# Optimization experiments

Hardware: AMD Instinct MI355X
Metric: run time of the kernel (lower is better)

The kernel has to match this reference:

```python
import jax, jax.numpy as jnp
import numpy as np

LN_EPS = 1e-5
LOG_EPS = 1e-8

def _layernorm(x, w, b):
    mu = jnp.mean(x, axis=-1, keepdims=True)
    var = jnp.mean((x - mu) ** 2, axis=-1, keepdims=True)
    return (x - mu) * jax.lax.rsqrt(var + LN_EPS) * w + b


def setup_inputs() -> dict:
    key = jax.random.key(0)
    ks = jax.random.split(key, 8)
    B, T, D = 4, 4096, 1024
    x = jax.random.normal(ks[0], (B, T, D), dtype=jnp.float32)
    ln_w = jnp.ones((D,), jnp.float32)
    ln_b = jnp.zeros((D,), jnp.float32)
    # torch Linear stores weight as (out, in)
    Wf = jax.random.normal(ks[1], (D, D), jnp.float32) / np.sqrt(D)
    bf = jax.random.normal(ks[2], (D,), jnp.float32) * 0.02
    # module inits reach to zeros; use small random values for a non-trivial baseline
    Wr = jax.random.normal(ks[3], (D, D), jnp.float32) * 0.02
    br = jax.random.normal(ks[4], (D,), jnp.float32) * 0.02
    alpha_bias = jnp.array([3.0], jnp.float32) + jax.random.normal(ks[5], (1,), jnp.float32) * 0.1
    beta_scale = jnp.array([0.02], jnp.float32)
    return {"x": x, "ln_w": ln_w, "ln_b": ln_b, "Wf": Wf, "bf": bf,
            "Wr": Wr, "br": br, "alpha_bias": alpha_bias, "beta_scale": beta_scale}


def reference(x, ln_w, ln_b, Wf, bf, Wr, br, alpha_bias, beta_scale):
    residual = x
    x_norm = _layernorm(x, ln_w, ln_b)                       # [B,T,D]
    alpha = jax.nn.sigmoid(jnp.einsum('btd,ed->bte', x_norm, Wf) + bf + alpha_bias)
    beta_x = beta_scale * (1.0 - alpha) * x_norm
    log_alpha = jnp.log(alpha + LOG_EPS)
    log_alpha_cumsum = jnp.cumsum(log_alpha, axis=1)          # [B,T,D]
    m = jnp.max(log_alpha_cumsum, axis=1, keepdims=True)      # [B,1,D]
    scale = jnp.exp(log_alpha_cumsum - m)
    x_star = beta_x * scale
    s_star = jnp.cumsum(x_star, axis=1)
    output = s_star / (scale + LOG_EPS)
    x_gate = jnp.tanh(jnp.einsum('btd,ed->bte', output, Wr) + br)
    return x_gate * 0.05 + residual
```

## Files before the change

### kernel.cpp

```cpp
#include <hip/hip_runtime.h>

#define D_DIM 1024
#define B_DIM 4
#define T_DIM 4096
#define M_DIM (B_DIM * T_DIM)
#define CHUNK 32
#define NCHUNK (T_DIM / CHUNK)
#define NWAVE_C 16
#define SEG (NCHUNK / NWAVE_C)

typedef unsigned short u16;
typedef __attribute__((ext_vector_type(8))) unsigned short us8;
typedef __attribute__((ext_vector_type(8))) __bf16 bf16x8;
typedef __attribute__((ext_vector_type(4))) float f32x4;

__device__ __forceinline__ float bf2f(u16 u) {
    union { unsigned int i; float f; } v;
    v.i = ((unsigned int)u) << 16;
    return v.f;
}
__device__ __forceinline__ u16 f2bf(float f) {
    union { float f; unsigned int i; } v;
    v.f = f;
    unsigned int u = v.i;
    unsigned int r = (u + 0x7fffu + ((u >> 16) & 1u)) >> 16;
    return (u16)r;
}
__device__ __forceinline__ float fast_tanh(float v) {
    float e = __expf(2.f * v);
    return 1.f - 2.f / (e + 1.f);
}

#define GLOAD16(g, l)                                                   \
    __builtin_amdgcn_global_load_lds(                                   \
        (const __attribute__((address_space(1))) void*)(g),             \
        (__attribute__((address_space(3))) void*)(l), 16, 0, 0)

__global__ __launch_bounds__(256) void ln_conv_kernel(const float* __restrict__ x,
                                                      const float* __restrict__ w,
                                                      const float* __restrict__ b,
                                                      u16* __restrict__ xn,
                                                      const float* __restrict__ Wf,
                                                      const float* __restrict__ Wr,
                                                      u16* __restrict__ da,
                                                      u16* __restrict__ db) {
    __shared__ float red[8];
    int tid = threadIdx.x;
    if (blockIdx.x < 2048) {
        int i = blockIdx.x * 256 + tid;
        const float* s = (i < 262144) ? Wf : Wr;
        u16* dp = (i < 262144) ? da : db;
        int j = i & 262143;
        float4 v = ((const float4*)s)[j];
        ushort4 o;
        o.x = f2bf(v.x); o.y = f2bf(v.y); o.z = f2bf(v.z); o.w = f2bf(v.w);
        ((ushort4*)dp)[j] = o;
        return;
    }
    int row = blockIdx.x - 2048;
    float4 v = ((const float4*)(x + (size_t)row * D_DIM))[tid];
    float s  = v.x + v.y + v.z + v.w;
    float s2 = v.x * v.x + v.y * v.y + v.z * v.z + v.w * v.w;
    #pragma unroll
    for (int o = 32; o > 0; o >>= 1) {
        s  += __shfl_xor(s, o, 64);
        s2 += __shfl_xor(s2, o, 64);
    }
    int wave = tid >> 6, lane = tid & 63;
    if (lane == 0) { red[wave] = s; red[wave + 4] = s2; }
    __syncthreads();
    if (tid == 0) {
        float ts  = red[0] + red[1] + red[2] + red[3];
        float ts2 = red[4] + red[5] + red[6] + red[7];
        float mu  = ts * (1.0f / D_DIM);
        float var = ts2 * (1.0f / D_DIM) - mu * mu;
        red[0] = mu;
        red[1] = rsqrtf(var + 1e-5f);
    }
    __syncthreads();
    float mu = red[0], rs = red[1];
    float4 wv = ((const float4*)w)[tid];
    float4 bv = ((const float4*)b)[tid];
    ushort4 o;
    o.x = f2bf((v.x - mu) * rs * wv.x + bv.x);
    o.y = f2bf((v.y - mu) * rs * wv.y + bv.y);
    o.z = f2bf((v.z - mu) * rs * wv.z + bv.z);
    o.w = f2bf((v.w - mu) * rs * wv.w + bv.w);
    ((ushort4*)(xn + (size_t)row * D_DIM))[tid] = o;
}

template <int EPI>
__global__ __launch_bounds__(256) void gemm_kernel(const u16* __restrict__ A,
                                                   const u16* __restrict__ Bm,
                                                   const float* __restrict__ bias,
                                                   const float* __restrict__ resid,
                                                   const float* __restrict__ sc0,
                                                   u16* __restrict__ out_bf,
                                                   float* __restrict__ out_f) {
    __shared__ __align__(16) u16 lds_a[128 * 32];
    __shared__ __align__(16) u16 lds_b[128 * 32];
    int tid  = threadIdx.x;
    int wave = tid >> 6, lane = tid & 63;
    int tile_n = blockIdx.x * 128;
    int tile_m = blockIdx.y * 128;
    int wr = wave >> 1, wc = wave & 1;

    f32x4 acc[4][4] = {};

    int srow = wave * 32 + (lane >> 2);
    int scol = (lane & 3) * 8;
    const u16* ga0 = A  + (size_t)(tile_m + srow) * D_DIM + scol;
    const u16* ga1 = ga0 + 16 * D_DIM;
    const u16* gb0 = Bm + (size_t)(tile_n + srow) * D_DIM + scol;
    const u16* gb1 = gb0 + 16 * D_DIM;
    u16* la0 = &lds_a[(wave * 32) * 32];
    u16* la1 = &lds_a[(wave * 32 + 16) * 32];
    u16* lb0 = &lds_b[(wave * 32) * 32];
    u16* lb1 = &lds_b[(wave * 32 + 16) * 32];

    for (int k0 = 0; k0 < D_DIM; k0 += 32) {
        GLOAD16(ga0 + k0, la0);
        GLOAD16(ga1 + k0, la1);
        GLOAD16(gb0 + k0, lb0);
        GLOAD16(gb1 + k0, lb1);
        __syncthreads();

        bf16x8 af[4], bfr[4];
        #pragma unroll
        for (int mi = 0; mi < 4; mi++) {
            int m = wr * 64 + mi * 16 + (lane & 15);
            af[mi] = *(const bf16x8*)&lds_a[m * 32 + (lane >> 4) * 8];
        }
        #pragma unroll
        for (int ni = 0; ni < 4; ni++) {
            int n = wc * 64 + ni * 16 + (lane & 15);
            bfr[ni] = *(const bf16x8*)&lds_b[n * 32 + (lane >> 4) * 8];
        }
        #pragma unroll
        for (int mi = 0; mi < 4; mi++)
            #pragma unroll
            for (int ni = 0; ni < 4; ni++)
                acc[mi][ni] = __builtin_amdgcn_mfma_f32_16x16x32_bf16(
                    af[mi], bfr[ni], acc[mi][ni], 0, 0, 0);
        __syncthreads();
    }

    if constexpr (EPI == 0) {
        float abv = sc0[0];
        #pragma unroll
        for (int mi = 0; mi < 4; mi++) {
            #pragma unroll
            for (int r = 0; r < 4; r++) {
                int row = tile_m + wr * 64 + mi * 16 + (lane >> 4) * 4 + r;
                #pragma unroll
                for (int ni = 0; ni < 4; ni++) {
                    int col = tile_n + wc * 64 + ni * 16 + (lane & 15);
                    size_t idx = (size_t)row * D_DIM + col;
                    float z = acc[mi][ni][r] + bias[col] + abv;
                    float alpha = 1.f / (1.f + __expf(-z));
                    out_bf[idx] = f2bf(__logf(alpha + 1e-8f));
                }
            }
        }
    } else {
        #pragma unroll
        for (int mi = 0; mi < 4; mi++) {
            #pragma unroll
            for (int r = 0; r < 4; r++) {
                int row = tile_m + wr * 64 + mi * 16 + (lane >> 4) * 4 + r;
                #pragma unroll
                for (int ni = 0; ni < 4; ni++) {
                    int col = tile_n + wc * 64 + ni * 16 + (lane & 15);
                    size_t idx = (size_t)row * D_DIM + col;
                    float g = fast_tanh(acc[mi][ni][r] + bias[col]);
                    out_f[idx] = 0.05f * g + resid[idx];
                }
            }
        }
    }
}

__global__ __launch_bounds__(256) void scan_chunk(const u16* __restrict__ la,
                                                  const u16* __restrict__ xn,
                                                  const float* __restrict__ bs,
                                                  float* __restrict__ S,
                                                  float* __restrict__ Ml,
                                                  float* __restrict__ Tb) {
    int bc = blockIdx.x;
    int b = bc >> 7, c = bc & (NCHUNK - 1);
    int col0 = threadIdx.x * 4;
    float bsv = bs[0];
    size_t base = ((size_t)(b * T_DIM + c * CHUNK)) * D_DIM + col0;
    float run[4], mx[4];
    #pragma unroll
    for (int j = 0; j < 4; j++) { run[j] = 0.f; mx[j] = -3.4e38f; }
    #pragma unroll 4
    for (int t = 0; t < CHUNK; t++) {
        ushort4 v = *(const ushort4*)(la + base + (size_t)t * D_DIM);
        run[0] += bf2f(v.x); mx[0] = fmaxf(mx[0], run[0]);
        run[1] += bf2f(v.y); mx[1] = fmaxf(mx[1], run[1]);
        run[2] += bf2f(v.z); mx[2] = fmaxf(mx[2], run[2]);
        run[3] += bf2f(v.w); mx[3] = fmaxf(mx[3], run[3]);
    }
    float tb[4], p[4];
    #pragma unroll
    for (int j = 0; j < 4; j++) { tb[j] = 0.f; p[j] = 0.f; }
    #pragma unroll 4
    for (int t = 0; t < CHUNK; t++) {
        size_t idx = base + (size_t)t * D_DIM;
        ushort4 lv = *(const ushort4*)(la + idx);
        ushort4 xv = *(const ushort4*)(xn + idx);
        u16 lvs[4] = {lv.x, lv.y, lv.z, lv.w};
        u16 xvs[4] = {xv.x, xv.y, xv.z, xv.w};
        #pragma unroll
        for (int j = 0; j < 4; j++) {
            float lav = bf2f(lvs[j]);
            p[j] += lav;
            float bx = bsv * (1.f - __expf(lav)) * bf2f(xvs[j]);
            tb[j] += bx * __expf(p[j] - mx[j]);
        }
    }
    size_t ci = ((size_t)(b * NCHUNK + c)) * D_DIM + col0;
    #pragma unroll
    for (int j = 0; j < 4; j++) { S[ci + j] = run[j]; Ml[ci + j] = mx[j]; Tb[ci + j] = tb[j]; }
}

__global__ __launch_bounds__(1024) void scan_combine(const float* __restrict__ S,
                                                     const float* __restrict__ Ml,
                                                     const float* __restrict__ Tb,
                                                     float* __restrict__ Of,
                                                     float* __restrict__ SSp) {
    __shared__ float lsS[NWAVE_C][64], lsM[NWAVE_C][64], lsW[NWAVE_C][64];
    int b = blockIdx.x >> 4;
    int dg = blockIdx.x & 15;
    int wave = threadIdx.x >> 6, lane = threadIdx.x & 63;
    int d = dg * 64 + lane;
    size_t base = ((size_t)b * NCHUNK) * D_DIM + d;
    int c0 = wave * SEG;

    float O = 0.f, m = -3.4e38f;
    #pragma unroll
    for (int j = 0; j < SEG; j++) {
        size_t ci = base + (size_t)(c0 + j) * D_DIM;
        m = fmaxf(m, O + Ml[ci]);
        O += S[ci];
    }
    lsS[wave][lane] = O; lsM[wave][lane] = m;
    __syncthreads();

    float myOsup = 0.f, gm = -3.4e38f;
    {
        float o = 0.f;
        #pragma unroll
        for (int w2 = 0; w2 < NWAVE_C; w2++) {
            if (w2 == wave) myOsup = o;
            gm = fmaxf(gm, o + lsM[w2][lane]);
            o += lsS[w2][lane];
        }
    }

    float wv[SEG];
    float wacc = 0.f, Oc = myOsup;
    #pragma unroll
    for (int j = 0; j < SEG; j++) {
        size_t ci = base + (size_t)(c0 + j) * D_DIM;
        Of[ci] = Oc - gm;
        float wcj = __expf(Oc + Ml[ci] - gm) * Tb[ci];
        wv[j] = wacc;
        wacc += wcj;
        Oc += S[ci];
    }
    lsW[wave][lane] = wacc;
    __syncthreads();

    float ssup = 0.f;
    #pragma unroll
    for (int w2 = 0; w2 < NWAVE_C; w2++)
        if (w2 < wave) ssup += lsW[w2][lane];

    #pragma unroll
    for (int j = 0; j < SEG; j++) {
        size_t ci = base + (size_t)(c0 + j) * D_DIM;
        SSp[ci] = ssup + wv[j];
    }
}

__global__ __launch_bounds__(256) void scan_final(const u16* __restrict__ la,
                                                  const u16* __restrict__ xn,
                                                  const float* __restrict__ bs,
                                                  const float* __restrict__ Of,
                                                  const float* __restrict__ SSp,
                                                  u16* __restrict__ osc) {
    int bc = blockIdx.x;
    int b = bc >> 7, c = bc & (NCHUNK - 1);
    int col0 = threadIdx.x * 4;
    float bsv = bs[0];
    size_t base = ((size_t)(b * T_DIM + c * CHUNK)) * D_DIM + col0;
    size_t ci = ((size_t)(b * NCHUNK + c)) * D_DIM + col0;
    float ofs[4], ss[4], p[4];
    #pragma unroll
    for (int j = 0; j < 4; j++) { ofs[j] = Of[ci + j]; ss[j] = SSp[ci + j]; p[j] = 0.f; }
    #pragma unroll 4
    for (int t = 0; t < CHUNK; t++) {
        size_t idx = base + (size_t)t * D_DIM;
        ushort4 lv = *(const ushort4*)(la + idx);
        ushort4 xv = *(const ushort4*)(xn + idx);
        u16 lvs[4] = {lv.x, lv.y, lv.z, lv.w};
        u16 xvs[4] = {xv.x, xv.y, xv.z, xv.w};
        ushort4 o;
        u16 os[4];
        #pragma unroll
        for (int j = 0; j < 4; j++) {
            float lav = bf2f(lvs[j]);
            p[j] += lav;
            float scv = __expf(ofs[j] + p[j]);
            float bx = bsv * (1.f - __expf(lav)) * bf2f(xvs[j]);
            ss[j] += bx * scv;
            os[j] = f2bf(ss[j] / (scv + 1e-8f));
        }
        o.x = os[0]; o.y = os[1]; o.z = os[2]; o.w = os[3];
        *(ushort4*)(osc + idx) = o;
    }
}

extern "C" void kernel_launch(void* const* d_in, const int* in_sizes, int n_in,
                              void* d_out, int out_size, void* d_ws, size_t ws_size,
                              hipStream_t stream) {
    const float* x   = (const float*)d_in[0];
    const float* lnw = (const float*)d_in[1];
    const float* lnb = (const float*)d_in[2];
    const float* Wf  = (const float*)d_in[3];
    const float* bf_ = (const float*)d_in[4];
    const float* Wr  = (const float*)d_in[5];
    const float* br  = (const float*)d_in[6];
    const float* ab  = (const float*)d_in[7];
    const float* bs  = (const float*)d_in[8];
    float* out = (float*)d_out;

    char* w = (char*)d_ws;
    u16* xn  = (u16*)w;
    u16* la  = (u16*)(w + (size_t)33554432);
    u16* Wfc = (u16*)(w + (size_t)67108864);
    u16* Wrc = (u16*)(w + (size_t)69206016);
    float* S   = (float*)(w + (size_t)71303168);
    float* Ml  = S  + 524288;
    float* Tb  = Ml + 524288;
    float* Of  = Tb + 524288;
    float* SSp = Of + 524288;
    u16* osc = xn;

    ln_conv_kernel<<<dim3(2048 + M_DIM), dim3(256), 0, stream>>>(
        x, lnw, lnb, xn, Wf, Wr, Wfc, Wrc);
    gemm_kernel<0><<<dim3(D_DIM / 128, M_DIM / 128), dim3(256), 0, stream>>>(
        xn, Wfc, bf_, nullptr, ab, la, nullptr);
    scan_chunk<<<dim3(B_DIM * NCHUNK), dim3(256), 0, stream>>>(la, xn, bs, S, Ml, Tb);
    scan_combine<<<dim3(B_DIM * 16), dim3(1024), 0, stream>>>(S, Ml, Tb, Of, SSp);
    scan_final<<<dim3(B_DIM * NCHUNK), dim3(256), 0, stream>>>(la, xn, bs, Of, SSp, osc);
    gemm_kernel<1><<<dim3(D_DIM / 128, M_DIM / 128), dim3(256), 0, stream>>>(
        osc, Wrc, br, x, nullptr, nullptr, out);
}
```

Measured before the change: 308.1 us.

## Fuse chunk-scan summaries into first GEMM epilogue and simplify scan combine

The first GEMM epilogue now computes per-chunk sums of log-alpha and the weighted beta_x totals directly from accumulator registers, using cross-lane shuffles, and writes them out. This removes the separate scan_chunk kernel and its two extra passes over la and xn. The per-chunk max is replaced by using the first row's log-alpha as the stabilising offset, which drops the Ml buffer but could lose numerical stability if the cumulative sums drift far from that value. LayerNorm is also restructured to one row per wave, with shuffle-only reductions and no block syncs.

```diff
diff --git a/kernel.cpp b/kernel.cpp
--- a/kernel.cpp
+++ b/kernel.cpp
@@ -10,7 +10,6 @@
 #define SEG (NCHUNK / NWAVE_C)
 
 typedef unsigned short u16;
-typedef __attribute__((ext_vector_type(8))) unsigned short us8;
 typedef __attribute__((ext_vector_type(8))) __bf16 bf16x8;
 typedef __attribute__((ext_vector_type(4))) float f32x4;
 
@@ -44,7 +43,6 @@
                                                       const float* __restrict__ Wr,
                                                       u16* __restrict__ da,
                                                       u16* __restrict__ db) {
-    __shared__ float red[8];
     int tid = threadIdx.x;
     if (blockIdx.x < 2048) {
         int i = blockIdx.x * 256 + tid;
@@ -57,46 +55,49 @@
         ((ushort4*)dp)[j] = o;
         return;
     }
-    int row = blockIdx.x - 2048;
-    float4 v = ((const float4*)(x + (size_t)row * D_DIM))[tid];
-    float s  = v.x + v.y + v.z + v.w;
-    float s2 = v.x * v.x + v.y * v.y + v.z * v.z + v.w * v.w;
-    #pragma unroll
-    for (int o = 32; o > 0; o >>= 1) {
+    int wv = tid >> 6, lane = tid & 63;
+    int row = (blockIdx.x - 2048) * 4 + wv;
+    const float4* xr = (const float4*)(x + (size_t)row * D_DIM);
+    float4 xv[4];
+    #pragma unroll
+    for (int k = 0; k < 4; k++) xv[k] = xr[lane + 64 * k];
+    float s = 0.f, s2 = 0.f;
+    #pragma unroll
+    for (int k = 0; k < 4; k++) {
+        s  += xv[k].x + xv[k].y + xv[k].z + xv[k].w;
+        s2 += xv[k].x * xv[k].x + xv[k].y * xv[k].y
+            + xv[k].z * xv[k].z + xv[k].w * xv[k].w;
+    }
+    #pragma unroll
+    for (int o = 1; o < 64; o <<= 1) {
         s  += __shfl_xor(s, o, 64);
         s2 += __shfl_xor(s2, o, 64);
     }
-    int wave = tid >> 6, lane = tid & 63;
-    if (lane == 0) { red[wave] = s; red[wave + 4] = s2; }
-    __syncthreads();
-    if (tid == 0) {
-        float ts  = red[0] + red[1] + red[2] + red[3];
-        float ts2 = red[4] + red[5] + red[6] + red[7];
-        float mu  = ts * (1.0f / D_DIM);
-        float var = ts2 * (1.0f / D_DIM) - mu * mu;
-        red[0] = mu;
-        red[1] = rsqrtf(var + 1e-5f);
-    }
-    __syncthreads();
-    float mu = red[0], rs = red[1];
-    float4 wv = ((const float4*)w)[tid];
-    float4 bv = ((const float4*)b)[tid];
-    ushort4 o;
-    o.x = f2bf((v.x - mu) * rs * wv.x + bv.x);
-    o.y = f2bf((v.y - mu) * rs * wv.y + bv.y);
-    o.z = f2bf((v.z - mu) * rs * wv.z + bv.z);
-    o.w = f2bf((v.w - mu) * rs * wv.w + bv.w);
-    ((ushort4*)(xn + (size_t)row * D_DIM))[tid] = o;
-}
-
-template <int EPI>
-__global__ __launch_bounds__(256) void gemm_kernel(const u16* __restrict__ A,
-                                                   const u16* __restrict__ Bm,
-                                                   const float* __restrict__ bias,
-                                                   const float* __restrict__ resid,
-                                                   const float* __restrict__ sc0,
-                                                   u16* __restrict__ out_bf,
-                                                   float* __restrict__ out_f) {
+    float mu = s * (1.0f / D_DIM);
+    float var = s2 * (1.0f / D_DIM) - mu * mu;
+    float rs = rsqrtf(var + 1e-5f);
+    ushort4* xo = (ushort4*)(xn + (size_t)row * D_DIM);
+    #pragma unroll
+    for (int k = 0; k < 4; k++) {
+        float4 wv4 = ((const float4*)w)[lane + 64 * k];
+        float4 bv4 = ((const float4*)b)[lane + 64 * k];
+        ushort4 o;
+        o.x = f2bf((xv[k].x - mu) * rs * wv4.x + bv4.x);
+        o.y = f2bf((xv[k].y - mu) * rs * wv4.y + bv4.y);
+        o.z = f2bf((xv[k].z - mu) * rs * wv4.z + bv4.z);
+        o.w = f2bf((xv[k].w - mu) * rs * wv4.w + bv4.w);
+        xo[lane + 64 * k] = o;
+    }
+}
+
+__global__ __launch_bounds__(256) void gemm1_kernel(const u16* __restrict__ xn,
+                                                    const u16* __restrict__ Wfc,
+                                                    const float* __restrict__ bf_,
+                                                    const float* __restrict__ ab,
+                                                    const float* __restrict__ bs,
+                                                    u16* __restrict__ out_la,
+                                                    float* __restrict__ Sg,
+                                                    float* __restrict__ Tg) {
     __shared__ __align__(16) u16 lds_a[128 * 32];
     __shared__ __align__(16) u16 lds_b[128 * 32];
     int tid  = threadIdx.x;
@@ -104,14 +105,13 @@
     int tile_n = blockIdx.x * 128;
     int tile_m = blockIdx.y * 128;
     int wr = wave >> 1, wc = wave & 1;
-
     f32x4 acc[4][4] = {};
 
     int srow = wave * 32 + (lane >> 2);
     int scol = (lane & 3) * 8;
-    const u16* ga0 = A  + (size_t)(tile_m + srow) * D_DIM + scol;
+    const u16* ga0 = xn  + (size_t)(tile_m + srow) * D_DIM + scol;
     const u16* ga1 = ga0 + 16 * D_DIM;
-    const u16* gb0 = Bm + (size_t)(tile_n + srow) * D_DIM + scol;
+    const u16* gb0 = Wfc + (size_t)(tile_n + srow) * D_DIM + scol;
     const u16* gb1 = gb0 + 16 * D_DIM;
     u16* la0 = &lds_a[(wave * 32) * 32];
     u16* la1 = &lds_a[(wave * 32 + 16) * 32];
@@ -124,7 +124,6 @@
         GLOAD16(gb0 + k0, lb0);
         GLOAD16(gb1 + k0, lb1);
         __syncthreads();
-
         bf16x8 af[4], bfr[4];
         #pragma unroll
         for (int mi = 0; mi < 4; mi++) {
@@ -145,143 +144,98 @@
         __syncthreads();
     }
 
-    if constexpr (EPI == 0) {
-        float abv = sc0[0];
-        #pragma unroll
-        for (int mi = 0; mi < 4; mi++) {
-            #pragma unroll
-            for (int r = 0; r < 4; r++) {
-                int row = tile_m + wr * 64 + mi * 16 + (lane >> 4) * 4 + r;
+    float abv = ab[0], bsv = bs[0];
+    int q = lane >> 4, l = lane & 15;
+    #pragma unroll
+    for (int ni = 0; ni < 4; ni++) {
+        int col = tile_n + wc * 64 + ni * 16 + l;
+        float bcol = bf_[col];
+        #pragma unroll
+        for (int ch = 0; ch < 2; ch++) {
+            float lav[2][4], bxv[2][4];
+            #pragma unroll
+            for (int h = 0; h < 2; h++) {
+                int mi = 2 * ch + h;
                 #pragma unroll
-                for (int ni = 0; ni < 4; ni++) {
-                    int col = tile_n + wc * 64 + ni * 16 + (lane & 15);
-                    size_t idx = (size_t)row * D_DIM + col;
-                    float z = acc[mi][ni][r] + bias[col] + abv;
+                for (int r = 0; r < 4; r++) {
+                    int row = tile_m + wr * 64 + mi * 16 + q * 4 + r;
+                    float z = acc[mi][ni][r] + bcol + abv;
                     float alpha = 1.f / (1.f + __expf(-z));
-                    out_bf[idx] = f2bf(__logf(alpha + 1e-8f));
+                    float la_ = __logf(alpha + 1e-8f);
+                    float xv = bf2f(xn[(size_t)row * D_DIM + col]);
+                    lav[h][r] = la_;
+                    bxv[h][r] = bsv * (1.f - alpha) * xv;
+                    out_la[(size_t)row * D_DIM + col] = f2bf(la_);
                 }
             }
-        }
-    } else {
-        #pragma unroll
-        for (int mi = 0; mi < 4; mi++) {
-            #pragma unroll
-            for (int r = 0; r < 4; r++) {
-                int row = tile_m + wr * 64 + mi * 16 + (lane >> 4) * 4 + r;
-                #pragma unroll
-                for (int ni = 0; ni < 4; ni++) {
-                    int col = tile_n + wc * 64 + ni * 16 + (lane & 15);
-                    size_t idx = (size_t)row * D_DIM + col;
-                    float g = fast_tanh(acc[mi][ni][r] + bias[col]);
-                    out_f[idx] = 0.05f * g + resid[idx];
-                }
+            float s0 = lav[0][0] + lav[0][1] + lav[0][2] + lav[0][3];
+            float s1 = lav[1][0] + lav[1][1] + lav[1][2] + lav[1][3];
+            float x0 = s0, x1 = s1, y;
+            y = __shfl_up(x0, 16, 64); if (q >= 1) x0 += y;
+            y = __shfl_up(x0, 32, 64); if (q >= 2) x0 += y;
+            y = __shfl_up(x1, 16, 64); if (q >= 1) x1 += y;
+            y = __shfl_up(x1, 32, 64); if (q >= 2) x1 += y;
+            float t0 = __shfl(x0, l + 48, 64);
+            float t1 = __shfl(x1, l + 48, 64);
+            float e0 = x0 - s0, e1 = x1 - s1;
+            float pr = e0, Tp = 0.f;
+            #pragma unroll
+            for (int r = 0; r < 4; r++) { pr += lav[0][r]; Tp += bxv[0][r] * __expf(pr); }
+            pr = t0 + e1;
+            #pragma unroll
+            for (int r = 0; r < 4; r++) { pr += lav[1][r]; Tp += bxv[1][r] * __expf(pr); }
+            Tp += __shfl_xor(Tp, 16, 64);
+            Tp += __shfl_xor(Tp, 32, 64);
+            if (q == 0) {
+                int cidx = (tile_m >> 5) + wr * 2 + ch;
+                Sg[(size_t)cidx * D_DIM + col] = t0 + t1;
+                Tg[(size_t)cidx * D_DIM + col] = Tp;
             }
         }
     }
 }
 
-__global__ __launch_bounds__(256) void scan_chunk(const u16* __restrict__ la,
-                                                  const u16* __restrict__ xn,
-                                                  const float* __restrict__ bs,
-                                                  float* __restrict__ S,
-                                                  float* __restrict__ Ml,
-                                                  float* __restrict__ Tb) {
-    int bc = blockIdx.x;
-    int b = bc >> 7, c = bc & (NCHUNK - 1);
-    int col0 = threadIdx.x * 4;
-    float bsv = bs[0];
-    size_t base = ((size_t)(b * T_DIM + c * CHUNK)) * D_DIM + col0;
-    float run[4], mx[4];
-    #pragma unroll
-    for (int j = 0; j < 4; j++) { run[j] = 0.f; mx[j] = -3.4e38f; }
-    #pragma unroll 4
-    for (int t = 0; t < CHUNK; t++) {
-        ushort4 v = *(const ushort4*)(la + base + (size_t)t * D_DIM);
-        run[0] += bf2f(v.x); mx[0] = fmaxf(mx[0], run[0]);
-        run[1] += bf2f(v.y); mx[1] = fmaxf(mx[1], run[1]);
-        run[2] += bf2f(v.z); mx[2] = fmaxf(mx[2], run[2]);
-        run[3] += bf2f(v.w); mx[3] = fmaxf(mx[3], run[3]);
-    }
-    float tb[4], p[4];
-    #pragma unroll
-    for (int j = 0; j < 4; j++) { tb[j] = 0.f; p[j] = 0.f; }
-    #pragma unroll 4
-    for (int t = 0; t < CHUNK; t++) {
-        size_t idx = base + (size_t)t * D_DIM;
-        ushort4 lv = *(const ushort4*)(la + idx);
-        ushort4 xv = *(const ushort4*)(xn + idx);
-        u16 lvs[4] = {lv.x, lv.y, lv.z, lv.w};
-        u16 xvs[4] = {xv.x, xv.y, xv.z, xv.w};
-        #pragma unroll
-        for (int j = 0; j < 4; j++) {
-            float lav = bf2f(lvs[j]);
-            p[j] += lav;
-            float bx = bsv * (1.f - __expf(lav)) * bf2f(xvs[j]);
-            tb[j] += bx * __expf(p[j] - mx[j]);
-        }
-    }
-    size_t ci = ((size_t)(b * NCHUNK + c)) * D_DIM + col0;
-    #pragma unroll
-    for (int j = 0; j < 4; j++) { S[ci + j] = run[j]; Ml[ci + j] = mx[j]; Tb[ci + j] = tb[j]; }
-}
-
-__global__ __launch_bounds__(1024) void scan_combine(const float* __restrict__ S,
-                                                     const float* __restrict__ Ml,
+__global__ __launch_bounds__(1024) void scan_combine(const u16* __restrict__ la,
+                                                     const float* __restrict__ S,
                                                      const float* __restrict__ Tb,
                                                      float* __restrict__ Of,
                                                      float* __restrict__ SSp) {
-    __shared__ float lsS[NWAVE_C][64], lsM[NWAVE_C][64], lsW[NWAVE_C][64];
+    __shared__ float lsS[NWAVE_C][64], lsW[NWAVE_C][64];
     int b = blockIdx.x >> 4;
     int dg = blockIdx.x & 15;
     int wave = threadIdx.x >> 6, lane = threadIdx.x & 63;
     int d = dg * 64 + lane;
+    float m = bf2f(la[(size_t)(b * T_DIM) * D_DIM + d]);
     size_t base = ((size_t)b * NCHUNK) * D_DIM + d;
     int c0 = wave * SEG;
 
-    float O = 0.f, m = -3.4e38f;
+    float OfR[SEG], wR[SEG];
+    float Or = 0.f, w = 0.f;
     #pragma unroll
     for (int j = 0; j < SEG; j++) {
         size_t ci = base + (size_t)(c0 + j) * D_DIM;
-        m = fmaxf(m, O + Ml[ci]);
-        O += S[ci];
-    }
-    lsS[wave][lane] = O; lsM[wave][lane] = m;
+        OfR[j] = Or;
+        wR[j]  = w;
+        w  += __expf(Or) * Tb[ci];
+        Or += S[ci];
+    }
+    lsS[wave][lane] = Or; lsW[wave][lane] = w;
     __syncthreads();
 
-    float myOsup = 0.f, gm = -3.4e38f;
-    {
-        float o = 0.f;
-        #pragma unroll
-        for (int w2 = 0; w2 < NWAVE_C; w2++) {
-            if (w2 == wave) myOsup = o;
-            gm = fmaxf(gm, o + lsM[w2][lane]);
-            o += lsS[w2][lane];
-        }
-    }
-
-    float wv[SEG];
-    float wacc = 0.f, Oc = myOsup;
+    float o = 0.f, s = 0.f, myO = 0.f, myS = 0.f;
+    #pragma unroll
+    for (int w2 = 0; w2 < NWAVE_C; w2++) {
+        if (w2 == wave) { myO = o; myS = s; }
+        s += __expf(o - m) * lsW[w2][lane];
+        o += lsS[w2][lane];
+    }
+
+    float em = __expf(myO - m);
     #pragma unroll
     for (int j = 0; j < SEG; j++) {
         size_t ci = base + (size_t)(c0 + j) * D_DIM;
-        Of[ci] = Oc - gm;
-        float wcj = __expf(Oc + Ml[ci] - gm) * Tb[ci];
-        wv[j] = wacc;
-        wacc += wcj;
-        Oc += S[ci];
-    }
-    lsW[wave][lane] = wacc;
-    __syncthreads();
-
-    float ssup = 0.f;
-    #pragma unroll
-    for (int w2 = 0; w2 < NWAVE_C; w2++)
-        if (w2 < wave) ssup += lsW[w2][lane];
-
-    #pragma unroll
-    for (int j = 0; j < SEG; j++) {
-        size_t ci = base + (size_t)(c0 + j) * D_DIM;
-        SSp[ci] = ssup + wv[j];
+        Of[ci]  = myO + OfR[j] - m;
+        SSp[ci] = myS + em * wR[j];
     }
 }
 
@@ -300,14 +254,13 @@
     float ofs[4], ss[4], p[4];
     #pragma unroll
     for (int j = 0; j < 4; j++) { ofs[j] = Of[ci + j]; ss[j] = SSp[ci + j]; p[j] = 0.f; }
-    #pragma unroll 4
+    #pragma unroll 8
     for (int t = 0; t < CHUNK; t++) {
         size_t idx = base + (size_t)t * D_DIM;
         ushort4 lv = *(const ushort4*)(la + idx);
         ushort4 xv = *(const ushort4*)(xn + idx);
         u16 lvs[4] = {lv.x, lv.y, lv.z, lv.w};
         u16 xvs[4] = {xv.x, xv.y, xv.z, xv.w};
-        ushort4 o;
         u16 os[4];
         #pragma unroll
         for (int j = 0; j < 4; j++) {
@@ -318,8 +271,72 @@
             ss[j] += bx * scv;
             os[j] = f2bf(ss[j] / (scv + 1e-8f));
         }
-        o.x = os[0]; o.y = os[1]; o.z = os[2]; o.w = os[3];
+        ushort4 o; o.x = os[0]; o.y = os[1]; o.z = os[2]; o.w = os[3];
         *(ushort4*)(osc + idx) = o;
+    }
+}
+
+__global__ __launch_bounds__(256) void gemm2_kernel(const u16* __restrict__ A,
+                                                    const u16* __restrict__ Bm,
+                                                    const float* __restrict__ bias,
+                                                    const float* __restrict__ resid,
+                                                    float* __restrict__ out_f) {
+    __shared__ __align__(16) u16 lds_a[128 * 32];
+    __shared__ __align__(16) u16 lds_b[128 * 32];
+    int tid  = threadIdx.x;
+    int wave = tid >> 6, lane = tid & 63;
+    int tile_n = blockIdx.x * 128;
+    int tile_m = blockIdx.y * 128;
+    int wr = wave >> 1, wc = wave & 1;
+    f32x4 acc[4][4] = {};
+    int srow = wave * 32 + (lane >> 2);
+    int scol = (lane & 3) * 8;
+    const u16* ga0 = A  + (size_t)(tile_m + srow) * D_DIM + scol;
+    const u16* ga1 = ga0 + 16 * D_DIM;
+    const u16* gb0 = Bm + (size_t)(tile_n + srow) * D_DIM + scol;
+    const u16* gb1 = gb0 + 16 * D_DIM;
+    u16* la0 = &lds_a[(wave * 32) * 32];
+    u16* la1 = &lds_a[(wave * 32 + 16) * 32];
+    u16* lb0 = &lds_b[(wave * 32) * 32];
+    u16* lb1 = &lds_b[(wave * 32 + 16) * 32];
+    for (int k0 = 0; k0 < D_DIM; k0 += 32) {
+        GLOAD16(ga0 + k0, la0);
+        GLOAD16(ga1 + k0, la1);
+        GLOAD16(gb0 + k0, lb0);
+        GLOAD16(gb1 + k0, lb1);
+        __syncthreads();
+        bf16x8 af[4], bfr[4];
+        #pragma unroll
+        for (int mi = 0; mi < 4; mi++) {
+            int m = wr * 64 + mi * 16 + (lane & 15);
+            af[mi] = *(const bf16x8*)&lds_a[m * 32 + (lane >> 4) * 8];
+        }
+        #pragma unroll
+        for (int ni = 0; ni < 4; ni++) {
+            int n = wc * 64 + ni * 16 + (lane & 15);
+            bfr[ni] = *(const bf16x8*)&lds_b[n * 32 + (lane >> 4) * 8];
+        }
+        #pragma unroll
+        for (int mi = 0; mi < 4; mi++)
+            #pragma unroll
+            for (int ni = 0; ni < 4; ni++)
+                acc[mi][ni] = __builtin_amdgcn_mfma_f32_16x16x32_bf16(
+                    af[mi], bfr[ni], acc[mi][ni], 0, 0, 0);
+        __syncthreads();
+    }
+    #pragma unroll
+    for (int mi = 0; mi < 4; mi++) {
+        #pragma unroll
+        for (int r = 0; r < 4; r++) {
+            int row = tile_m + wr * 64 + mi * 16 + (lane >> 4) * 4 + r;
+            #pragma unroll
+            for (int ni = 0; ni < 4; ni++) {
+                int col = tile_n + wc * 64 + ni * 16 + (lane & 15);
+                size_t idx = (size_t)row * D_DIM + col;
+                float g = fast_tanh(acc[mi][ni][r] + bias[col]);
+                out_f[idx] = 0.05f * g + resid[idx];
+            }
+        }
     }
 }
 
@@ -343,19 +360,17 @@
     u16* Wfc = (u16*)(w + (size_t)67108864);
     u16* Wrc = (u16*)(w + (size_t)69206016);
     float* S   = (float*)(w + (size_t)71303168);
-    float* Ml  = S  + 524288;
-    float* Tb  = Ml + 524288;
+    float* Tb  = S  + 524288;
     float* Of  = Tb + 524288;
     float* SSp = Of + 524288;
     u16* osc = xn;
 
-    ln_conv_kernel<<<dim3(2048 + M_DIM), dim3(256), 0, stream>>>(
+    ln_conv_kernel<<<dim3(2048 + M_DIM / 4), dim3(256), 0, stream>>>(
         x, lnw, lnb, xn, Wf, Wr, Wfc, Wrc);
-    gemm_kernel<0><<<dim3(D_DIM / 128, M_DIM / 128), dim3(256), 0, stream>>>(
-        xn, Wfc, bf_, nullptr, ab, la, nullptr);
-    scan_chunk<<<dim3(B_DIM * NCHUNK), dim3(256), 0, stream>>>(la, xn, bs, S, Ml, Tb);
-    scan_combine<<<dim3(B_DIM * 16), dim3(1024), 0, stream>>>(S, Ml, Tb, Of, SSp);
+    gemm1_kernel<<<dim3(D_DIM / 128, M_DIM / 128), dim3(256), 0, stream>>>(
+        xn, Wfc, bf_, ab, bs, la, S, Tb);
+    scan_combine<<<dim3(B_DIM * 16), dim3(1024), 0, stream>>>(la, S, Tb, Of, SSp);
     scan_final<<<dim3(B_DIM * NCHUNK), dim3(256), 0, stream>>>(la, xn, bs, Of, SSp, osc);
-    gemm_kernel<1><<<dim3(D_DIM / 128, M_DIM / 128), dim3(256), 0, stream>>>(
-        osc, Wrc, br, x, nullptr, nullptr, out);
-}
+    gemm2_kernel<<<dim3(D_DIM / 128, M_DIM / 128), dim3(256), 0, stream>>>(
+        osc, Wrc, br, x, out);
+}
```

Result: faster. 295.8 us (-4.0%).
